# Optimization experiments

Hardware: AMD Instinct MI355X
Metric: run time of the kernel (lower is better)

## Reference

```python
import jax, jax.numpy as jnp
import numpy as np

NUM_HEADS = 12
DIM = 768
HEAD_DIM = DIM // NUM_HEADS


def setup_inputs() -> dict:
    key = jax.random.key(0)
    k1, k2, k3, k4 = jax.random.split(key, 4)
    B, N, C = 4, 8192, DIM
    x = jax.random.normal(k1, (B, N, C), dtype=jnp.float32)
    # torch nn.Linear stores weight as (out_features, in_features)
    W_qkv = jax.random.normal(k2, (3 * C, C), dtype=jnp.float32) * (1.0 / np.sqrt(C))
    W_proj = jax.random.normal(k3, (C, C), dtype=jnp.float32) * (1.0 / np.sqrt(C))
    b_proj = jax.random.normal(k4, (C,), dtype=jnp.float32) * 0.01
    return {"x": x, "W_qkv": W_qkv, "W_proj": W_proj, "b_proj": b_proj}


def reference(x, W_qkv, W_proj, b_proj):
    B, N, C = x.shape
    H, D = NUM_HEADS, HEAD_DIM
    qkv = x @ W_qkv.T                                  # [B,N,3C]
    qkv = qkv.reshape(B, N, 3, H, D).transpose(2, 0, 3, 1, 4)  # [3,B,H,N,D]
    q, k, v = qkv[0], qkv[1], qkv[2]
    q = jax.nn.elu(q) + 1.0
    k = jax.nn.elu(k) + 1.0
    k_sum = k.sum(axis=-2)                             # [B,H,D]
    kv = jnp.einsum('bhnd,bhne->bhde', k, v)           # [B,H,D,D]
    numerator = jnp.einsum('bhnd,bhde->bhne', q, kv)   # [B,H,N,D]
    denominator = jnp.einsum('bhnd,bhd->bhn', q, k_sum)
    out = numerator / (denominator[..., None] + 1e-6)
    out = out.transpose(0, 2, 1, 3).reshape(B, N, C)   # [B,N,C]
    out = out @ W_proj.T + b_proj
    return out
```

## Files before the change

### kernel.cpp

```cpp
#include <hip/hip_runtime.h>
#include <hip/hip_bf16.h>
#include <stdint.h>

typedef __attribute__((ext_vector_type(8))) short short8;
typedef __attribute__((ext_vector_type(4))) float floatx4;
typedef __attribute__((ext_vector_type(16))) float floatx16;

#define NB 4
#define NN 8192
#define NC 768
#define NH 12
#define ND 64
#define LDQKV 2304
#define NSPLIT 16

__device__ __forceinline__ float bf2f(ushort u) {
    union { float f; uint32_t i; } x; x.i = ((uint32_t)u) << 16; return x.f;
}
__device__ __forceinline__ ushort f2bf(float f) {
    union { float f; uint32_t i; } x; x.f = f;
    uint32_t r = x.i + 0x7fff + ((x.i >> 16) & 1);
    return (ushort)(r >> 16);
}
typedef const __attribute__((address_space(1))) uint32_t* gas1_t;
typedef __attribute__((address_space(3))) uint32_t* las3_t;
__device__ __forceinline__ void gl_lds16(const void* g, const void* l) {
    __builtin_amdgcn_global_load_lds((gas1_t)(uintptr_t)g,
                                     (las3_t)(uint32_t)(uintptr_t)l, 16, 0, 0);
}

__global__ __launch_bounds__(256) void cvt_all(const float* __restrict__ X,
                                               const float* __restrict__ Wq,
                                               const float* __restrict__ Wp,
                                               ushort* __restrict__ xbf,
                                               ushort* __restrict__ wqbf,
                                               ushort* __restrict__ wpbf) {
    const int nx = 32768 * 768, nwq = 2304 * 768, nwp = 768 * 768;
    int i = (blockIdx.x * 256 + threadIdx.x) * 8;
    const float* src; ushort* dst;
    if (i < nx)            { src = X + i;              dst = xbf + i; }
    else if (i < nx + nwq) { i -= nx;  src = Wq + i;   dst = wqbf + i; }
    else                   { i -= nx + nwq; if (i >= nwp) return; src = Wp + i; dst = wpbf + i; }
    const float4 a = *(const float4*)src;
    const float4 b = *(const float4*)(src + 4);
    short8 v;
    v[0] = (short)f2bf(a.x); v[1] = (short)f2bf(a.y);
    v[2] = (short)f2bf(a.z); v[3] = (short)f2bf(a.w);
    v[4] = (short)f2bf(b.x); v[5] = (short)f2bf(b.y);
    v[6] = (short)f2bf(b.z); v[7] = (short)f2bf(b.w);
    *(short8*)dst = v;
}

template<int LDC, bool ELU, bool BIAS, typename OutT>
__global__ __launch_bounds__(256) void gemm_bt(const ushort* __restrict__ A,
                                               const ushort* __restrict__ Bw,
                                               const float* __restrict__ bias,
                                               OutT* __restrict__ Cout, int K) {
    __shared__ ushort As[128 * 32];
    __shared__ ushort Bs[128 * 32];
    const int t = threadIdx.x;
    const int w = t >> 6, lane = t & 63, l32 = lane & 31, hi = lane >> 5;
    const int wm = w & 1, wn = w >> 1;
    const int m0 = blockIdx.y * 128, n0 = blockIdx.x * 128;

    floatx16 acc[2][2] = {};

    const int rowA = t >> 2, chA = (t & 3) ^ (rowA & 3);
    const ushort* gA = A  + (size_t)(m0 + rowA) * K + chA * 8;
    const ushort* gB = Bw + (size_t)(n0 + rowA) * K + chA * 8;

    for (int k0 = 0; k0 < K; k0 += 32) {
        gl_lds16(gA + k0,                  As + w * 512);
        gl_lds16(gA + k0 + 64 * (size_t)K, As + 2048 + w * 512);
        gl_lds16(gB + k0,                  Bs + w * 512);
        gl_lds16(gB + k0 + 64 * (size_t)K, Bs + 2048 + w * 512);
        __syncthreads();
        short8 af[2][2], bfr[2][2];
        #pragma unroll
        for (int mt = 0; mt < 2; mt++)
            #pragma unroll
            for (int kh = 0; kh < 2; kh++) {
                const int row = wm * 64 + mt * 32 + l32;
                const int kc = kh * 2 + hi;
                af[mt][kh] = *(const short8*)&As[(row * 4 + (kc ^ (row & 3))) * 8];
            }
        #pragma unroll
        for (int nt = 0; nt < 2; nt++)
            #pragma unroll
            for (int kh = 0; kh < 2; kh++) {
                const int row = wn * 64 + nt * 32 + l32;
                const int kc = kh * 2 + hi;
                bfr[nt][kh] = *(const short8*)&Bs[(row * 4 + (kc ^ (row & 3))) * 8];
            }
        #pragma unroll
        for (int mt = 0; mt < 2; mt++)
            #pragma unroll
            for (int nt = 0; nt < 2; nt++)
                #pragma unroll
                for (int kh = 0; kh < 2; kh++)
                    acc[mt][nt] = __builtin_amdgcn_mfma_f32_32x32x16_bf16(
                        af[mt][kh], bfr[nt][kh], acc[mt][nt], 0, 0, 0);
        __syncthreads();
    }

    #pragma unroll
    for (int mt = 0; mt < 2; mt++)
        #pragma unroll
        for (int nt = 0; nt < 2; nt++) {
            const int col = n0 + wn * 64 + nt * 32 + l32;
            float bval = 0.f;
            if (BIAS) bval = bias[col];
            #pragma unroll
            for (int reg = 0; reg < 16; reg++) {
                const int row = m0 + wm * 64 + mt * 32 + (reg & 3) + 8 * (reg >> 2) + 4 * hi;
                float v = acc[mt][nt][reg];
                if (ELU) { if (col < 2 * NC) v = (v > 0.f) ? v + 1.f : __expf(v); }
                if (BIAS) v += bval;
                if (sizeof(OutT) == 2) Cout[(size_t)row * LDC + col] = (OutT)f2bf(v);
                else                   Cout[(size_t)row * LDC + col] = (OutT)v;
            }
        }
}

__global__ __launch_bounds__(256) void kv_ksum(const ushort* __restrict__ qkv,
                                               float* __restrict__ kvpart,
                                               float* __restrict__ kspart) {
    __shared__ ushort klds[128 * 64];
    __shared__ ushort vlds[128 * 64];
    __shared__ float  kvred[64 * 64];
    __shared__ float  ksred[4][64];
    const int bh = blockIdx.y, b = bh / NH, h = bh % NH;
    const int t = threadIdx.x, w = t >> 6, lane = t & 63, l16 = lane & 15, quad = lane >> 4;
    const int n0 = blockIdx.x * 512;
    const ushort* kbase = qkv + (size_t)(b * NN) * LDQKV + NC     + h * ND;
    const ushort* vbase = qkv + (size_t)(b * NN) * LDQKV + 2 * NC + h * ND;

    floatx4 acc[4][4] = {};
    floatx4 acc5[4] = {};
    short8 ones;
    #pragma unroll
    for (int j = 0; j < 8; j++) ones[j] = (l16 == 0) ? (short)0x3F80 : (short)0;

    const int rowT = t >> 3, ch = t & 7;

    for (int s = 0; s < 4; s++) {
        const int nb = n0 + s * 128;
        #pragma unroll
        for (int i = 0; i < 4; i++) {
            const size_t r = (size_t)(nb + i * 32 + rowT) * LDQKV + ch * 8;
            gl_lds16(kbase + r, klds + i * 2048 + w * 512);
            gl_lds16(vbase + r, vlds + i * 2048 + w * 512);
        }
        __syncthreads();
        short8 af[4], bfr[4];
        #pragma unroll
        for (int dt = 0; dt < 4; dt++) {
            short8 v;
            #pragma unroll
            for (int j = 0; j < 8; j++)
                v[j] = (short)klds[(w * 32 + quad * 8 + j) * 64 + dt * 16 + l16];
            af[dt] = v;
        }
        #pragma unroll
        for (int et = 0; et < 4; et++) {
            short8 v;
            #pragma unroll
            for (int j = 0; j < 8; j++)
                v[j] = (short)vlds[(w * 32 + quad * 8 + j) * 64 + et * 16 + l16];
            bfr[et] = v;
        }
        #pragma unroll
        for (int dt = 0; dt < 4; dt++) {
            #pragma unroll
            for (int et = 0; et < 4; et++)
                acc[dt][et] = __builtin_amdgcn_mfma_f32_16x16x32_bf16(af[dt], bfr[et], acc[dt][et], 0, 0, 0);
            acc5[dt] = __builtin_amdgcn_mfma_f32_16x16x32_bf16(af[dt], ones, acc5[dt], 0, 0, 0);
        }
        __syncthreads();
    }

    if (w == 0) {
        #pragma unroll
        for (int dt = 0; dt < 4; dt++)
            #pragma unroll
            for (int et = 0; et < 4; et++)
                #pragma unroll
                for (int r = 0; r < 4; r++)
                    kvred[(dt * 16 + quad * 4 + r) * 64 + et * 16 + l16] = acc[dt][et][r];
    }
    if (l16 == 0) {
        #pragma unroll
        for (int dt = 0; dt < 4; dt++)
            #pragma unroll
            for (int r = 0; r < 4; r++)
                ksred[w][dt * 16 + quad * 4 + r] = acc5[dt][r];
    }
    __syncthreads();
    if (w != 0) {
        #pragma unroll
        for (int dt = 0; dt < 4; dt++)
            #pragma unroll
            for (int et = 0; et < 4; et++)
                #pragma unroll
                for (int r = 0; r < 4; r++)
                    atomicAdd(&kvred[(dt * 16 + quad * 4 + r) * 64 + et * 16 + l16], acc[dt][et][r]);
    }
    __syncthreads();
    float* kvp = kvpart + ((size_t)blockIdx.x * 48 + bh) * 4096;
    for (int i = t; i < 4096; i += 256) kvp[i] = kvred[i];
    if (t < 64) kspart[((size_t)blockIdx.x * 48 + bh) * 64 + t] =
        ksred[0][t] + ksred[1][t] + ksred[2][t] + ksred[3][t];
}

__global__ __launch_bounds__(256) void reduce_kvks(const float* __restrict__ kvpart,
                                                   const float* __restrict__ kspart,
                                                   float* __restrict__ kvfinal,
                                                   float* __restrict__ ksfinal) {
    const int bh = blockIdx.y, t = threadIdx.x;
    if (blockIdx.x < 16) {
        const int i = blockIdx.x * 256 + t;
        float s = 0.f;
        #pragma unroll
        for (int p = 0; p < NSPLIT; p++) s += kvpart[((size_t)p * 48 + bh) * 4096 + i];
        kvfinal[(size_t)bh * 4096 + i] = s;
    } else if (t < 64) {
        float s = 0.f;
        #pragma unroll
        for (int p = 0; p < NSPLIT; p++) s += kspart[((size_t)p * 48 + bh) * 64 + t];
        ksfinal[bh * 64 + t] = s;
    }
}

__global__ __launch_bounds__(256) void attn_apply(const ushort* __restrict__ qkv,
                                                  const float* __restrict__ kvfinal,
                                                  const float* __restrict__ ksfinal,
                                                  ushort* __restrict__ outpre) {
    __shared__ ushort kvb[64 * 80];
    const int bh = blockIdx.y, b = bh / NH, h = bh % NH;
    const int t = threadIdx.x, w = t >> 6, lane = t & 63, l16 = lane & 15, quad = lane >> 4;

    for (int i = t; i < 4096; i += 256) {
        const int d = i >> 6, e = i & 63;
        kvb[d * 80 + e] = f2bf(kvfinal[(size_t)bh * 4096 + i]);
    }
    for (int i = t; i < 1024; i += 256) {
        const int d = i >> 4, c = i & 15;
        kvb[d * 80 + 64 + c] = (c == 0) ? f2bf(ksfinal[bh * 64 + d]) : (ushort)0;
    }
    __syncthreads();

    short8 bfr[5][2];
    #pragma unroll
    for (int et = 0; et < 5; et++)
        #pragma unroll
        for (int ks = 0; ks < 2; ks++) {
            short8 v;
            #pragma unroll
            for (int j = 0; j < 8; j++)
                v[j] = (short)kvb[(ks * 32 + quad * 8 + j) * 80 + et * 16 + l16];
            bfr[et][ks] = v;
        }

    const ushort* qbase = qkv + (size_t)(b * NN) * LDQKV + h * ND;
    ushort* obase = outpre + (size_t)(b * NN) * NC + h * ND;
    const int n0 = blockIdx.x * 512;

    for (int it = 0; it < 8; it++) {
        const int nt = n0 + (it * 4 + w) * 16;
        const ushort* qp = qbase + (size_t)(nt + l16) * LDQKV + quad * 8;
        const short8 a0 = *(const short8*)qp;
        const short8 a1 = *(const short8*)(qp + 32);
        floatx4 acc[5] = {};
        #pragma unroll
        for (int et = 0; et < 5; et++) {
            acc[et] = __builtin_amdgcn_mfma_f32_16x16x32_bf16(a0, bfr[et][0], acc[et], 0, 0, 0);
            acc[et] = __builtin_amdgcn_mfma_f32_16x16x32_bf16(a1, bfr[et][1], acc[et], 0, 0, 0);
        }
        float dv[4];
        #pragma unroll
        for (int r = 0; r < 4; r++) dv[r] = __shfl(acc[4][r], lane & 48);
        #pragma unroll
        for (int et = 0; et < 4; et++)
            #pragma unroll
            for (int r = 0; r < 4; r++) {
                const float o = acc[et][r] / (dv[r] + 1e-6f);
                obase[(size_t)(nt + quad * 4 + r) * NC + et * 16 + l16] = f2bf(o);
            }
    }
}

extern "C" void kernel_launch(void* const* d_in, const int* in_sizes, int n_in,
                              void* d_out, int out_size, void* d_ws, size_t ws_size,
                              hipStream_t stream) {
    (void)in_sizes; (void)n_in; (void)out_size; (void)ws_size;
    const float* X     = (const float*)d_in[0];
    const float* Wqkv  = (const float*)d_in[1];
    const float* Wproj = (const float*)d_in[2];
    const float* bproj = (const float*)d_in[3];
    float* out = (float*)d_out;

    char* ws = (char*)d_ws;
    size_t off = 0;
    ushort* qkv     = (ushort*)(ws + off); off += (size_t)32768 * 2304 * 2;
    ushort* outpre  = (ushort*)(ws + off); off += (size_t)32768 * 768 * 2;
    ushort* xbf     = (ushort*)(ws + off); off += (size_t)32768 * 768 * 2;
    ushort* wqkvbf  = (ushort*)(ws + off); off += (size_t)2304 * 768 * 2;
    ushort* wprojbf = (ushort*)(ws + off); off += (size_t)768 * 768 * 2;
    float* kvpart  = (float*)xbf;
    float* kspart  = kvpart + (size_t)NSPLIT * 48 * 4096;
    float* kvfinal = kspart + (size_t)NSPLIT * 48 * 64;
    float* ksfinal = kvfinal + (size_t)48 * 4096;

    const int ncvt = (32768 * 768 + 2304 * 768 + 768 * 768) / 8 / 256;
    cvt_all<<<ncvt, 256, 0, stream>>>(X, Wqkv, Wproj, xbf, wqkvbf, wprojbf);

    gemm_bt<LDQKV, true, false, ushort><<<dim3(18, 256), 256, 0, stream>>>(xbf, wqkvbf, nullptr, qkv, NC);
    kv_ksum<<<dim3(NSPLIT, 48), 256, 0, stream>>>(qkv, kvpart, kspart);
    reduce_kvks<<<dim3(17, 48), 256, 0, stream>>>(kvpart, kspart, kvfinal, ksfinal);
    attn_apply<<<dim3(NSPLIT, 48), 256, 0, stream>>>(qkv, kvfinal, ksfinal, outpre);
    gemm_bt<NC, false, true, float><<<dim3(6, 256), 256, 0, stream>>>(outpre, wprojbf, bproj, out, NC);
}
```

Measured before the change: 503.5 us.

## Write K and V transposed from QKV GEMM and swizzle kv_ksum LDS reads

The QKV GEMM epilogue now splits its output into a row-major Q buffer and transposed K and V buffers (feature-major over tokens), written as packed 4-element stores. This lets kv_ksum load K and V tiles with XOR-swizzled LDS layout and read MFMA fragments as single 16-byte vector loads instead of eight scalar strided LDS reads. Both GEMMs also get a 1D grid with a grouped block order intended to improve L2 reuse. The risk is that the transposed epilogue stores from the GEMM are less coalesced than the previous row-major writes.

```diff
diff --git a/kernel.cpp b/kernel.cpp
--- a/kernel.cpp
+++ b/kernel.cpp
@@ -3,6 +3,7 @@
 #include <stdint.h>
 
 typedef __attribute__((ext_vector_type(8))) short short8;
+typedef __attribute__((ext_vector_type(4))) short short4v;
 typedef __attribute__((ext_vector_type(4))) float floatx4;
 typedef __attribute__((ext_vector_type(16))) float floatx16;
 
@@ -11,7 +12,7 @@
 #define NC 768
 #define NH 12
 #define ND 64
-#define LDQKV 2304
+#define MTOT 32768
 #define NSPLIT 16
 
 __device__ __forceinline__ float bf2f(ushort u) {
@@ -35,7 +36,7 @@
                                                ushort* __restrict__ xbf,
                                                ushort* __restrict__ wqbf,
                                                ushort* __restrict__ wpbf) {
-    const int nx = 32768 * 768, nwq = 2304 * 768, nwp = 768 * 768;
+    const int nx = MTOT * NC, nwq = 3 * NC * NC, nwp = NC * NC;
     int i = (blockIdx.x * 256 + threadIdx.x) * 8;
     const float* src; ushort* dst;
     if (i < nx)            { src = X + i;              dst = xbf + i; }
@@ -51,17 +52,20 @@
     *(short8*)dst = v;
 }
 
-template<int LDC, bool ELU, bool BIAS, typename OutT>
-__global__ __launch_bounds__(256) void gemm_bt(const ushort* __restrict__ A,
-                                               const ushort* __restrict__ Bw,
-                                               const float* __restrict__ bias,
-                                               OutT* __restrict__ Cout, int K) {
+__global__ __launch_bounds__(256) void gemm_qkv(const ushort* __restrict__ A,
+                                                const ushort* __restrict__ Bw,
+                                                ushort* __restrict__ qbuf,
+                                                ushort* __restrict__ kT,
+                                                ushort* __restrict__ vT) {
+    const int K = NC;
     __shared__ ushort As[128 * 32];
     __shared__ ushort Bs[128 * 32];
     const int t = threadIdx.x;
     const int w = t >> 6, lane = t & 63, l32 = lane & 31, hi = lane >> 5;
     const int wm = w & 1, wn = w >> 1;
-    const int m0 = blockIdx.y * 128, n0 = blockIdx.x * 128;
+    const int bx = blockIdx.x;
+    const int m0 = ((bx & 7) + 8 * ((bx >> 3) & 31)) * 128;
+    const int n0 = (bx >> 8) * 128;
 
     floatx16 acc[2][2] = {};
 
@@ -108,32 +112,116 @@
         #pragma unroll
         for (int nt = 0; nt < 2; nt++) {
             const int col = n0 + wn * 64 + nt * 32 + l32;
-            float bval = 0.f;
-            if (BIAS) bval = bias[col];
+            const int rbase = m0 + wm * 64 + mt * 32 + 4 * hi;
+            if (col < NC) {
+                #pragma unroll
+                for (int reg = 0; reg < 16; reg++) {
+                    const int row = rbase + (reg & 3) + 8 * (reg >> 2);
+                    float v = acc[mt][nt][reg];
+                    v = (v > 0.f) ? v + 1.f : __expf(v);
+                    qbuf[(size_t)row * NC + col] = f2bf(v);
+                }
+            } else {
+                const bool isK = col < 2 * NC;
+                ushort* dst = isK ? (kT + (size_t)(col - NC) * MTOT)
+                                  : (vT + (size_t)(col - 2 * NC) * MTOT);
+                #pragma unroll
+                for (int rq = 0; rq < 4; rq++) {
+                    short4v pk;
+                    #pragma unroll
+                    for (int r = 0; r < 4; r++) {
+                        float v = acc[mt][nt][rq * 4 + r];
+                        if (isK) v = (v > 0.f) ? v + 1.f : __expf(v);
+                        pk[r] = (short)f2bf(v);
+                    }
+                    *(short4v*)&dst[rbase + 8 * rq] = pk;
+                }
+            }
+        }
+}
+
+__global__ __launch_bounds__(256) void gemm_proj(const ushort* __restrict__ A,
+                                                 const ushort* __restrict__ Bw,
+                                                 const float* __restrict__ bias,
+                                                 float* __restrict__ Cout) {
+    const int K = NC;
+    __shared__ ushort As[128 * 32];
+    __shared__ ushort Bs[128 * 32];
+    const int t = threadIdx.x;
+    const int w = t >> 6, lane = t & 63, l32 = lane & 31, hi = lane >> 5;
+    const int wm = w & 1, wn = w >> 1;
+    const int bx = blockIdx.x;
+    const int m0 = ((bx & 7) + 8 * ((bx >> 3) & 31)) * 128;
+    const int n0 = (bx >> 8) * 128;
+
+    floatx16 acc[2][2] = {};
+
+    const int rowA = t >> 2, chA = (t & 3) ^ (rowA & 3);
+    const ushort* gA = A  + (size_t)(m0 + rowA) * K + chA * 8;
+    const ushort* gB = Bw + (size_t)(n0 + rowA) * K + chA * 8;
+
+    for (int k0 = 0; k0 < K; k0 += 32) {
+        gl_lds16(gA + k0,                  As + w * 512);
+        gl_lds16(gA + k0 + 64 * (size_t)K, As + 2048 + w * 512);
+        gl_lds16(gB + k0,                  Bs + w * 512);
+        gl_lds16(gB + k0 + 64 * (size_t)K, Bs + 2048 + w * 512);
+        __syncthreads();
+        short8 af[2][2], bfr[2][2];
+        #pragma unroll
+        for (int mt = 0; mt < 2; mt++)
+            #pragma unroll
+            for (int kh = 0; kh < 2; kh++) {
+                const int row = wm * 64 + mt * 32 + l32;
+                const int kc = kh * 2 + hi;
+                af[mt][kh] = *(const short8*)&As[(row * 4 + (kc ^ (row & 3))) * 8];
+            }
+        #pragma unroll
+        for (int nt = 0; nt < 2; nt++)
+            #pragma unroll
+            for (int kh = 0; kh < 2; kh++) {
+                const int row = wn * 64 + nt * 32 + l32;
+                const int kc = kh * 2 + hi;
+                bfr[nt][kh] = *(const short8*)&Bs[(row * 4 + (kc ^ (row & 3))) * 8];
+            }
+        #pragma unroll
+        for (int mt = 0; mt < 2; mt++)
+            #pragma unroll
+            for (int nt = 0; nt < 2; nt++)
+                #pragma unroll
+                for (int kh = 0; kh < 2; kh++)
+                    acc[mt][nt] = __builtin_amdgcn_mfma_f32_32x32x16_bf16(
+                        af[mt][kh], bfr[nt][kh], acc[mt][nt], 0, 0, 0);
+        __syncthreads();
+    }
+
+    #pragma unroll
+    for (int mt = 0; mt < 2; mt++)
+        #pragma unroll
+        for (int nt = 0; nt < 2; nt++) {
+            const int col = n0 + wn * 64 + nt * 32 + l32;
+            const float bval = bias[col];
+            const int rbase = m0 + wm * 64 + mt * 32 + 4 * hi;
             #pragma unroll
             for (int reg = 0; reg < 16; reg++) {
-                const int row = m0 + wm * 64 + mt * 32 + (reg & 3) + 8 * (reg >> 2) + 4 * hi;
-                float v = acc[mt][nt][reg];
-                if (ELU) { if (col < 2 * NC) v = (v > 0.f) ? v + 1.f : __expf(v); }
-                if (BIAS) v += bval;
-                if (sizeof(OutT) == 2) Cout[(size_t)row * LDC + col] = (OutT)f2bf(v);
-                else                   Cout[(size_t)row * LDC + col] = (OutT)v;
-            }
-        }
-}
-
-__global__ __launch_bounds__(256) void kv_ksum(const ushort* __restrict__ qkv,
+                const int row = rbase + (reg & 3) + 8 * (reg >> 2);
+                Cout[(size_t)row * NC + col] = acc[mt][nt][reg] + bval;
+            }
+        }
+}
+
+__global__ __launch_bounds__(256) void kv_ksum(const ushort* __restrict__ kT,
+                                               const ushort* __restrict__ vT,
                                                float* __restrict__ kvpart,
                                                float* __restrict__ kspart) {
-    __shared__ ushort klds[128 * 64];
-    __shared__ ushort vlds[128 * 64];
+    __shared__ ushort klds[64 * 128];
+    __shared__ ushort vlds[64 * 128];
     __shared__ float  kvred[64 * 64];
     __shared__ float  ksred[4][64];
     const int bh = blockIdx.y, b = bh / NH, h = bh % NH;
     const int t = threadIdx.x, w = t >> 6, lane = t & 63, l16 = lane & 15, quad = lane >> 4;
-    const int n0 = blockIdx.x * 512;
-    const ushort* kbase = qkv + (size_t)(b * NN) * LDQKV + NC     + h * ND;
-    const ushort* vbase = qkv + (size_t)(b * NN) * LDQKV + 2 * NC + h * ND;
+    const int T0 = b * NN + blockIdx.x * 512;
+    const ushort* kTb = kT + (size_t)(h * ND) * MTOT + T0;
+    const ushort* vTb = vT + (size_t)(h * ND) * MTOT + T0;
 
     floatx4 acc[4][4] = {};
     floatx4 acc5[4] = {};
@@ -141,33 +229,31 @@
     #pragma unroll
     for (int j = 0; j < 8; j++) ones[j] = (l16 == 0) ? (short)0x3F80 : (short)0;
 
-    const int rowT = t >> 3, ch = t & 7;
-
-    for (int s = 0; s < 4; s++) {
-        const int nb = n0 + s * 128;
+    const int rI = lane >> 4;
+    const int sI = lane & 15;
+
+    for (int tl = 0; tl < 4; tl++) {
         #pragma unroll
         for (int i = 0; i < 4; i++) {
-            const size_t r = (size_t)(nb + i * 32 + rowT) * LDQKV + ch * 8;
-            gl_lds16(kbase + r, klds + i * 2048 + w * 512);
-            gl_lds16(vbase + r, vlds + i * 2048 + w * 512);
+            const int r = i * 16 + w * 4 + rI;
+            const int cg = sI ^ (r & 7);
+            const size_t ga = (size_t)r * MTOT + tl * 128 + cg * 8;
+            gl_lds16(kTb + ga, klds + (i * 16 + w * 4) * 128);
+            gl_lds16(vTb + ga, vlds + (i * 16 + w * 4) * 128);
         }
         __syncthreads();
         short8 af[4], bfr[4];
         #pragma unroll
         for (int dt = 0; dt < 4; dt++) {
-            short8 v;
-            #pragma unroll
-            for (int j = 0; j < 8; j++)
-                v[j] = (short)klds[(w * 32 + quad * 8 + j) * 64 + dt * 16 + l16];
-            af[dt] = v;
+            const int r = dt * 16 + l16;
+            const int slot = (w * 4 + quad) ^ (r & 7);
+            af[dt] = *(const short8*)&klds[r * 128 + slot * 8];
         }
         #pragma unroll
         for (int et = 0; et < 4; et++) {
-            short8 v;
-            #pragma unroll
-            for (int j = 0; j < 8; j++)
-                v[j] = (short)vlds[(w * 32 + quad * 8 + j) * 64 + et * 16 + l16];
-            bfr[et] = v;
+            const int r = et * 16 + l16;
+            const int slot = (w * 4 + quad) ^ (r & 7);
+            bfr[et] = *(const short8*)&vlds[r * 128 + slot * 8];
         }
         #pragma unroll
         for (int dt = 0; dt < 4; dt++) {
@@ -231,7 +317,7 @@
     }
 }
 
-__global__ __launch_bounds__(256) void attn_apply(const ushort* __restrict__ qkv,
+__global__ __launch_bounds__(256) void attn_apply(const ushort* __restrict__ qbuf,
                                                   const float* __restrict__ kvfinal,
                                                   const float* __restrict__ ksfinal,
                                                   ushort* __restrict__ outpre) {
@@ -261,13 +347,13 @@
             bfr[et][ks] = v;
         }
 
-    const ushort* qbase = qkv + (size_t)(b * NN) * LDQKV + h * ND;
+    const ushort* qbase = qbuf + (size_t)(b * NN) * NC + h * ND;
     ushort* obase = outpre + (size_t)(b * NN) * NC + h * ND;
     const int n0 = blockIdx.x * 512;
 
     for (int it = 0; it < 8; it++) {
         const int nt = n0 + (it * 4 + w) * 16;
-        const ushort* qp = qbase + (size_t)(nt + l16) * LDQKV + quad * 8;
+        const ushort* qp = qbase + (size_t)(nt + l16) * NC + quad * 8;
         const short8 a0 = *(const short8*)qp;
         const short8 a1 = *(const short8*)(qp + 32);
         floatx4 acc[5] = {};
@@ -301,22 +387,24 @@
 
     char* ws = (char*)d_ws;
     size_t off = 0;
-    ushort* qkv     = (ushort*)(ws + off); off += (size_t)32768 * 2304 * 2;
-    ushort* outpre  = (ushort*)(ws + off); off += (size_t)32768 * 768 * 2;
-    ushort* xbf     = (ushort*)(ws + off); off += (size_t)32768 * 768 * 2;
-    ushort* wqkvbf  = (ushort*)(ws + off); off += (size_t)2304 * 768 * 2;
-    ushort* wprojbf = (ushort*)(ws + off); off += (size_t)768 * 768 * 2;
+    ushort* qbuf    = (ushort*)(ws + off); off += (size_t)MTOT * NC * 2;
+    ushort* kT      = (ushort*)(ws + off); off += (size_t)NC * MTOT * 2;
+    ushort* vT      = (ushort*)(ws + off); off += (size_t)NC * MTOT * 2;
+    ushort* outpre  = (ushort*)(ws + off); off += (size_t)MTOT * NC * 2;
+    ushort* xbf     = (ushort*)(ws + off); off += (size_t)MTOT * NC * 2;
+    ushort* wqkvbf  = (ushort*)(ws + off); off += (size_t)3 * NC * NC * 2;
+    ushort* wprojbf = (ushort*)(ws + off); off += (size_t)NC * NC * 2;
     float* kvpart  = (float*)xbf;
     float* kspart  = kvpart + (size_t)NSPLIT * 48 * 4096;
     float* kvfinal = kspart + (size_t)NSPLIT * 48 * 64;
     float* ksfinal = kvfinal + (size_t)48 * 4096;
 
-    const int ncvt = (32768 * 768 + 2304 * 768 + 768 * 768) / 8 / 256;
+    const int ncvt = (MTOT * NC + 3 * NC * NC + NC * NC) / 8 / 256;
     cvt_all<<<ncvt, 256, 0, stream>>>(X, Wqkv, Wproj, xbf, wqkvbf, wprojbf);
 
-    gemm_bt<LDQKV, true, false, ushort><<<dim3(18, 256), 256, 0, stream>>>(xbf, wqkvbf, nullptr, qkv, NC);
-    kv_ksum<<<dim3(NSPLIT, 48), 256, 0, stream>>>(qkv, kvpart, kspart);
+    gemm_qkv<<<4608, 256, 0, stream>>>(xbf, wqkvbf, qbuf, kT, vT);
+    kv_ksum<<<dim3(NSPLIT, 48), 256, 0, stream>>>(kT, vT, kvpart, kspart);
     reduce_kvks<<<dim3(17, 48), 256, 0, stream>>>(kvpart, kspart, kvfinal, ksfinal);
-    attn_apply<<<dim3(NSPLIT, 48), 256, 0, stream>>>(qkv, kvfinal, ksfinal, outpre);
-    gemm_bt<NC, false, true, float><<<dim3(6, 256), 256, 0, stream>>>(outpre, wprojbf, bproj, out, NC);
-}
+    attn_apply<<<dim3(NSPLIT, 48), 256, 0, stream>>>(qbuf, kvfinal, ksfinal, outpre);
+    gemm_proj<<<1536, 256, 0, stream>>>(outpre, wprojbf, bproj, out);
+}
```

Result: no change. 507.2 us (+0.7%).
